# Performance work log

Measured on AMD Instinct MI355X. Metric: run time of the kernel, lower is better.

The kernel has to match this reference:

```python
import jax, jax.numpy as jnp
import numpy as np

B = 2097152
CXR, ECG, EHR = 15, 14, 13
TOTAL = CXR + ECG + EHR  # 42
LN_EPS = 1e-5


def setup_inputs() -> dict:
    key = jax.random.key(0)
    ks = jax.random.split(key, 40)
    f32 = jnp.float32
    inp = {
        "cxr_probs": jax.random.normal(ks[0], (B, CXR), dtype=f32),
        "ecg_probs": jax.random.normal(ks[1], (B, ECG), dtype=f32),
        "ehr_probs": jax.random.normal(ks[2], (B, EHR), dtype=f32),
    }
    for i, (name, E) in enumerate([("cxr", CXR), ("ecg", ECG), ("ehr", EHR)]):
        k0 = 3 + i * 8
        s_in = 1.0 / np.sqrt(E)
        s_kv = 1.0 / np.sqrt(TOTAL)
        inp[f"in_w_{name}"] = jax.random.normal(ks[k0], (3 * E, E), dtype=f32) * s_in
        inp[f"in_b_{name}"] = jnp.zeros((3 * E,), dtype=f32)
        inp[f"out_w_{name}"] = jax.random.normal(ks[k0 + 1], (E, E), dtype=f32) * s_in
        inp[f"out_b_{name}"] = jnp.zeros((E,), dtype=f32)
        inp[f"kv_w_{name}"] = jax.random.normal(ks[k0 + 2], (E, TOTAL), dtype=f32) * s_kv
        inp[f"kv_b_{name}"] = jax.random.normal(ks[k0 + 3], (E,), dtype=f32) * s_kv
        inp[f"ln_g_{name}"] = jnp.ones((E,), dtype=f32)
        inp[f"ln_b_{name}"] = jnp.zeros((E,), dtype=f32)
    return inp


def _branch(x, ctx, in_w, in_b, out_w, out_b, kv_w, kv_b, ln_g, ln_b):
    # x: [B, E], ctx: [B, 42]
    E = x.shape[-1]
    kv = ctx @ kv_w.T + kv_b                      # [B, E]
    # nn.MultiheadAttention with q_len = kv_len = 1: softmax over a single
    # key is identically 1, so attn_out == v_proj(kv) exactly.
    Wv, bv = in_w[2 * E:], in_b[2 * E:]
    v = kv @ Wv.T + bv                            # [B, E]
    attended = v @ out_w.T + out_b                # [B, E]
    y = x + attended
    mu = jnp.mean(y, axis=-1, keepdims=True)
    var = jnp.mean(jnp.square(y - mu), axis=-1, keepdims=True)
    return (y - mu) * jax.lax.rsqrt(var + LN_EPS) * ln_g + ln_b


def reference(cxr_probs, ecg_probs, ehr_probs,
              in_w_cxr, in_b_cxr, out_w_cxr, out_b_cxr, kv_w_cxr, kv_b_cxr, ln_g_cxr, ln_b_cxr,
              in_w_ecg, in_b_ecg, out_w_ecg, out_b_ecg, kv_w_ecg, kv_b_ecg, ln_g_ecg, ln_b_ecg,
              in_w_ehr, in_b_ehr, out_w_ehr, out_b_ehr, kv_w_ehr, kv_b_ehr, ln_g_ehr, ln_b_ehr):
    ctx = jnp.concatenate([cxr_probs, ecg_probs, ehr_probs], axis=1)  # [B, 42]
    cxr_out = _branch(cxr_probs, ctx, in_w_cxr, in_b_cxr, out_w_cxr, out_b_cxr,
                      kv_w_cxr, kv_b_cxr, ln_g_cxr, ln_b_cxr)
    ecg_out = _branch(ecg_probs, ctx, in_w_ecg, in_b_ecg, out_w_ecg, out_b_ecg,
                      kv_w_ecg, kv_b_ecg, ln_g_ecg, ln_b_ecg)
    ehr_out = _branch(ehr_probs, ctx, in_w_ehr, in_b_ehr, out_w_ehr, out_b_ehr,
                      kv_w_ehr, kv_b_ehr, ln_g_ehr, ln_b_ehr)
    return (cxr_out, ecg_out, ehr_out)
```

## Files before the change

### kernel.cpp

```cpp
#include <hip/hip_runtime.h>
#include <stdint.h>

constexpr int CXR = 15, ECG = 14, EHR = 13;
constexpr int TOTAL = 42;
constexpr int MPITCH = 44;
constexpr float LN_EPS = 1e-5f;

constexpr int WS_M    = 0;
constexpr int WS_B    = TOTAL * MPITCH;
constexpr int WS_G    = WS_B + TOTAL;
constexpr int WS_BETA = WS_G + TOTAL;
constexpr int WS_FLOATS = WS_BETA + TOTAL;

constexpr int WROWS = 64;
constexpr int WFLOATS = WROWS * TOTAL;
constexpr int WS0F = 0;
constexpr int WS1F = WROWS * CXR;
constexpr int WS2F = WS1F + WROWS * ECG;
constexpr int WC0 = WROWS * CXR / 4;
constexpr int WC1 = WROWS * ECG / 4;
constexpr int WC2 = WROWS * EHR / 4;

typedef float f2v __attribute__((ext_vector_type(2)));
typedef __attribute__((address_space(4))) const f2v   CF2;
typedef __attribute__((address_space(4))) const float CFc;

__device__ __forceinline__ CF2* cast2(const float* p) {
    return (CF2*)(unsigned long long)p;
}
__device__ __forceinline__ CFc* cast1(const float* p) {
    return (CFc*)(unsigned long long)p;
}

struct FuseArgs {
    const float *in_w, *in_b, *out_w, *out_b, *kv_w, *kv_b, *ln_g, *ln_b;
    int E, R;
};

__global__ void fuse_weights_kernel(FuseArgs a0, FuseArgs a1, FuseArgs a2,
                                    float* __restrict__ ws) {
    FuseArgs a = (blockIdx.x == 0) ? a0 : (blockIdx.x == 1 ? a1 : a2);
    const int E = a.E, R = a.R;
    const int tid = threadIdx.x;

    __shared__ float T1[15 * 42];
    __shared__ float b1[15];

    for (int idx = tid; idx < E * TOTAL; idx += blockDim.x) {
        int i = idx / TOTAL, j = idx % TOTAL;
        float acc = 0.f;
        for (int k = 0; k < E; ++k)
            acc = fmaf(a.in_w[(2 * E + i) * E + k], a.kv_w[k * TOTAL + j], acc);
        T1[i * TOTAL + j] = acc;
    }
    if (tid < E) {
        float acc = a.in_b[2 * E + tid];
        for (int k = 0; k < E; ++k)
            acc = fmaf(a.in_w[(2 * E + tid) * E + k], a.kv_b[k], acc);
        b1[tid] = acc;
    }
    __syncthreads();

    for (int idx = tid; idx < E * MPITCH; idx += blockDim.x) {
        int i = idx / MPITCH, j = idx % MPITCH;
        float acc = 0.f;
        if (j < TOTAL)
            for (int k = 0; k < E; ++k)
                acc = fmaf(a.out_w[i * E + k], T1[k * TOTAL + j], acc);
        ws[WS_M + (R + i) * MPITCH + j] = acc;
    }
    if (tid < E) {
        float acc = a.out_b[tid];
        for (int k = 0; k < E; ++k)
            acc = fmaf(a.out_w[tid * E + k], b1[k], acc);
        ws[WS_B + R + tid]    = acc;
        ws[WS_G + R + tid]    = a.ln_g[tid];
        ws[WS_BETA + R + tid] = a.ln_b[tid];
    }
}

template <int CH>
__device__ __forceinline__ void stage_wave(const float* __restrict__ g,
                                           float* lds_seg_base, int lane) {
#pragma unroll
    for (int it = 0; it < (CH + 63) / 64; ++it) {
        int idx = lane + it * 64;
        if (idx < CH) {
            const __attribute__((address_space(1))) void* src =
                (const __attribute__((address_space(1))) void*)
                    ((const char*)g + (size_t)idx * 16);
            __attribute__((address_space(3))) void* dst =
                (__attribute__((address_space(3))) void*)
                    ((char*)lds_seg_base + it * 1024);
            __builtin_amdgcn_global_load_lds(src, dst, 16, 0, 0);
        }
    }
}

template <int E, int R, int SF>
__device__ __forceinline__ void compute_seg(const f2v (&ctx2)[MPITCH / 2],
                                            const float* __restrict__ ws,
                                            float* __restrict__ wb, int lane) {
    const float* ctxs = (const float*)ctx2;
    float y[E];
#pragma unroll
    for (int i = 0; i < E; ++i) {
        CF2* wrow = cast2(ws + WS_M + (R + i) * MPITCH);
        f2v acc = { *cast1(ws + WS_B + R + i), 0.f };
#pragma unroll
        for (int q = 0; q < MPITCH / 2; ++q) {
            f2v w = wrow[q];
            acc = __builtin_elementwise_fma(w, ctx2[q], acc);
        }
        y[i] = ctxs[R + i] + acc.x + acc.y;
    }
    float mu = 0.f;
#pragma unroll
    for (int i = 0; i < E; ++i) mu += y[i];
    mu *= (1.0f / E);
    float var = 0.f;
#pragma unroll
    for (int i = 0; i < E; ++i) { float d = y[i] - mu; var = fmaf(d, d, var); }
    var *= (1.0f / E);
    float rs = rsqrtf(var + LN_EPS);
#pragma unroll
    for (int i = 0; i < E; ++i) {
        float n = (y[i] - mu) * rs;
        wb[SF + lane * E + i] = fmaf(n, *cast1(ws + WS_G + R + i),
                                     *cast1(ws + WS_BETA + R + i));
    }
}

__global__ __launch_bounds__(128) void cmca_main(
        const float* __restrict__ cxr, const float* __restrict__ ecg,
        const float* __restrict__ ehr, const float* __restrict__ ws,
        float* __restrict__ out_cxr, float* __restrict__ out_ecg,
        float* __restrict__ out_ehr) {
    __shared__ __align__(16) float sbuf[2 * WFLOATS];
    const int tid = threadIdx.x;
    const int w = tid >> 6;
    const int lane = tid & 63;
    const size_t gw = (size_t)blockIdx.x * 2 + w;

    float* wb = sbuf + w * WFLOATS;

    const float* g0 = cxr + gw * (size_t)(WROWS * CXR);
    const float* g1 = ecg + gw * (size_t)(WROWS * ECG);
    const float* g2 = ehr + gw * (size_t)(WROWS * EHR);

    stage_wave<WC0>(g0, wb + WS0F, lane);
    stage_wave<WC1>(g1, wb + WS1F, lane);
    stage_wave<WC2>(g2, wb + WS2F, lane);
    asm volatile("s_waitcnt vmcnt(0)" ::: "memory");

    f2v ctx2[MPITCH / 2];
    float* ctxs = (float*)ctx2;
#pragma unroll
    for (int j = 0; j < CXR; ++j) ctxs[j] = wb[WS0F + lane * CXR + j];
#pragma unroll
    for (int j = 0; j < ECG; ++j) ctxs[CXR + j] = wb[WS1F + lane * ECG + j];
#pragma unroll
    for (int j = 0; j < EHR; ++j) ctxs[CXR + ECG + j] = wb[WS2F + lane * EHR + j];
    ctxs[42] = 0.f;
    ctxs[43] = 0.f;

    compute_seg<CXR, 0, WS0F>(ctx2, ws, wb, lane);
    compute_seg<ECG, CXR, WS1F>(ctx2, ws, wb, lane);
    compute_seg<EHR, CXR + ECG, WS2F>(ctx2, ws, wb, lane);

    const float4* wb4 = (const float4*)wb;
    float4* o0 = (float4*)(out_cxr + gw * (size_t)(WROWS * CXR));
    float4* o1 = (float4*)(out_ecg + gw * (size_t)(WROWS * ECG));
    float4* o2 = (float4*)(out_ehr + gw * (size_t)(WROWS * EHR));
#pragma unroll
    for (int it = 0; it < 4; ++it) {
        int idx = lane + it * 64;
        if (idx < WC0) o0[idx] = wb4[idx];
    }
#pragma unroll
    for (int it = 0; it < 4; ++it) {
        int idx = lane + it * 64;
        if (idx < WC1) o1[idx] = wb4[WC0 + idx];
    }
#pragma unroll
    for (int it = 0; it < 4; ++it) {
        int idx = lane + it * 64;
        if (idx < WC2) o2[idx] = wb4[WC0 + WC1 + idx];
    }
}

extern "C" void kernel_launch(void* const* d_in, const int* in_sizes, int n_in,
                              void* d_out, int out_size, void* d_ws, size_t ws_size,
                              hipStream_t stream) {
    const float* cxr = (const float*)d_in[0];
    const float* ecg = (const float*)d_in[1];
    const float* ehr = (const float*)d_in[2];
    float* ws = (float*)d_ws;
    float* out = (float*)d_out;

    const size_t Bn = (size_t)in_sizes[0] / CXR;

    auto mk = [&](int base, int E, int R) {
        FuseArgs a;
        a.in_w  = (const float*)d_in[base + 0];
        a.in_b  = (const float*)d_in[base + 1];
        a.out_w = (const float*)d_in[base + 2];
        a.out_b = (const float*)d_in[base + 3];
        a.kv_w  = (const float*)d_in[base + 4];
        a.kv_b  = (const float*)d_in[base + 5];
        a.ln_g  = (const float*)d_in[base + 6];
        a.ln_b  = (const float*)d_in[base + 7];
        a.E = E; a.R = R;
        return a;
    };
    FuseArgs a0 = mk(3, CXR, 0);
    FuseArgs a1 = mk(11, ECG, CXR);
    FuseArgs a2 = mk(19, EHR, CXR + ECG);

    fuse_weights_kernel<<<3, 256, 0, stream>>>(a0, a1, a2, ws);

    const int nblocks = (int)(Bn / (WROWS * 2));
    cmca_main<<<nblocks, 128, 0, stream>>>(cxr, ecg, ehr, ws,
                                           out,
                                           out + Bn * CXR,
                                           out + Bn * (CXR + ECG));
}
```

Measured before the change: 172.3 us.

## Compute fused 42x42 projection with fp16 MFMA instead of scalar FMAs

Adds a small kernel that packs the fused weight matrix, plus identity residual and bias row, into fp16 MFMA B-fragments. The main kernel converts each wave's 64 input rows to fp16 in a swizzled LDS arena and runs 16x16x32 f16 MFMAs. Accumulators are staged back through LDS for per-row LayerNorm. This removes the per-lane scalar FMA loop with its constant-memory weight reads, at the cost of fp16 rounding of inputs and weights, which risks accuracy, and extra LDS round-trips.

```diff
diff --git a/kernel.cpp b/kernel.cpp
--- a/kernel.cpp
+++ b/kernel.cpp
@@ -10,24 +10,16 @@
 constexpr int WS_B    = TOTAL * MPITCH;
 constexpr int WS_G    = WS_B + TOTAL;
 constexpr int WS_BETA = WS_G + TOTAL;
-constexpr int WS_FLOATS = WS_BETA + TOTAL;
+constexpr int WS_FRAG = 1976;
 
 constexpr int WROWS = 64;
-constexpr int WFLOATS = WROWS * TOTAL;
-constexpr int WS0F = 0;
-constexpr int WS1F = WROWS * CXR;
-constexpr int WS2F = WS1F + WROWS * ECG;
-constexpr int WC0 = WROWS * CXR / 4;
-constexpr int WC1 = WROWS * ECG / 4;
-constexpr int WC2 = WROWS * EHR / 4;
-
-typedef float f2v __attribute__((ext_vector_type(2)));
-typedef __attribute__((address_space(4))) const f2v   CF2;
+constexpr int ARENA_B = 11264;
+constexpr int S0F = 0, S1F = WROWS * CXR, S2F = S1F + WROWS * ECG;
+constexpr int WC0 = WROWS * CXR / 4, WC1 = WROWS * ECG / 4, WC2 = WROWS * EHR / 4;
+
+typedef _Float16 half8 __attribute__((ext_vector_type(8)));
+typedef float float4v __attribute__((ext_vector_type(4)));
 typedef __attribute__((address_space(4))) const float CFc;
-
-__device__ __forceinline__ CF2* cast2(const float* p) {
-    return (CF2*)(unsigned long long)p;
-}
 __device__ __forceinline__ CFc* cast1(const float* p) {
     return (CFc*)(unsigned long long)p;
 }
@@ -77,6 +69,31 @@
         ws[WS_G + R + tid]    = a.ln_g[tid];
         ws[WS_BETA + R + tid] = a.ln_b[tid];
     }
+}
+
+__global__ void fuse_frags_kernel(float* __restrict__ ws) {
+    const int tid = threadIdx.x;
+    if (tid >= 384) return;
+    const int l = tid & 63, nt = tid >> 6;
+    const int n = nt >> 1, t = nt & 1;
+    const int col = n * 16 + (l & 15);
+    const int k0 = t * 32 + 8 * (l >> 4);
+    half8 h;
+#pragma unroll
+    for (int i = 0; i < 8; ++i) {
+        int k = k0 + i;
+        float v = 0.f;
+        if (col < TOTAL) {
+            if (k < TOTAL) {
+                v = ws[WS_M + col * MPITCH + k];
+                if (k == col) v += 1.f;
+            } else if (k == TOTAL) {
+                v = ws[WS_B + col];
+            }
+        }
+        h[i] = (_Float16)v;
+    }
+    ((half8*)(ws + WS_FRAG))[nt * 64 + l] = h;
 }
 
 template <int CH>
@@ -97,81 +114,140 @@
     }
 }
 
-template <int E, int R, int SF>
-__device__ __forceinline__ void compute_seg(const f2v (&ctx2)[MPITCH / 2],
-                                            const float* __restrict__ ws,
-                                            float* __restrict__ wb, int lane) {
-    const float* ctxs = (const float*)ctx2;
-    float y[E];
-#pragma unroll
-    for (int i = 0; i < E; ++i) {
-        CF2* wrow = cast2(ws + WS_M + (R + i) * MPITCH);
-        f2v acc = { *cast1(ws + WS_B + R + i), 0.f };
-#pragma unroll
-        for (int q = 0; q < MPITCH / 2; ++q) {
-            f2v w = wrow[q];
-            acc = __builtin_elementwise_fma(w, ctx2[q], acc);
-        }
-        y[i] = ctxs[R + i] + acc.x + acc.y;
-    }
-    float mu = 0.f;
-#pragma unroll
-    for (int i = 0; i < E; ++i) mu += y[i];
-    mu *= (1.0f / E);
-    float var = 0.f;
-#pragma unroll
-    for (int i = 0; i < E; ++i) { float d = y[i] - mu; var = fmaf(d, d, var); }
-    var *= (1.0f / E);
-    float rs = rsqrtf(var + LN_EPS);
-#pragma unroll
-    for (int i = 0; i < E; ++i) {
-        float n = (y[i] - mu) * rs;
-        wb[SF + lane * E + i] = fmaf(n, *cast1(ws + WS_G + R + i),
-                                     *cast1(ws + WS_BETA + R + i));
-    }
-}
-
 __global__ __launch_bounds__(128) void cmca_main(
         const float* __restrict__ cxr, const float* __restrict__ ecg,
         const float* __restrict__ ehr, const float* __restrict__ ws,
         float* __restrict__ out_cxr, float* __restrict__ out_ecg,
         float* __restrict__ out_ehr) {
-    __shared__ __align__(16) float sbuf[2 * WFLOATS];
+    __shared__ __align__(16) char smem[2 * ARENA_B];
     const int tid = threadIdx.x;
-    const int w = tid >> 6;
-    const int lane = tid & 63;
+    const int w = tid >> 6, lane = tid & 63;
+    char* arena = smem + w * ARENA_B;
+    float* af = (float*)arena;
     const size_t gw = (size_t)blockIdx.x * 2 + w;
 
-    float* wb = sbuf + w * WFLOATS;
-
-    const float* g0 = cxr + gw * (size_t)(WROWS * CXR);
-    const float* g1 = ecg + gw * (size_t)(WROWS * ECG);
-    const float* g2 = ehr + gw * (size_t)(WROWS * EHR);
-
-    stage_wave<WC0>(g0, wb + WS0F, lane);
-    stage_wave<WC1>(g1, wb + WS1F, lane);
-    stage_wave<WC2>(g2, wb + WS2F, lane);
+    const half8* fr = (const half8*)(ws + WS_FRAG);
+    half8 bfrag[6];
+#pragma unroll
+    for (int q = 0; q < 6; ++q) bfrag[q] = fr[q * 64 + lane];
+
+    stage_wave<WC0>(cxr + gw * (size_t)(WROWS * CXR), af + S0F, lane);
+    stage_wave<WC1>(ecg + gw * (size_t)(WROWS * ECG), af + S1F, lane);
+    stage_wave<WC2>(ehr + gw * (size_t)(WROWS * EHR), af + S2F, lane);
     asm volatile("s_waitcnt vmcnt(0)" ::: "memory");
 
-    f2v ctx2[MPITCH / 2];
-    float* ctxs = (float*)ctx2;
-#pragma unroll
-    for (int j = 0; j < CXR; ++j) ctxs[j] = wb[WS0F + lane * CXR + j];
-#pragma unroll
-    for (int j = 0; j < ECG; ++j) ctxs[CXR + j] = wb[WS1F + lane * ECG + j];
-#pragma unroll
-    for (int j = 0; j < EHR; ++j) ctxs[CXR + ECG + j] = wb[WS2F + lane * EHR + j];
-    ctxs[42] = 0.f;
-    ctxs[43] = 0.f;
-
-    compute_seg<CXR, 0, WS0F>(ctx2, ws, wb, lane);
-    compute_seg<ECG, CXR, WS1F>(ctx2, ws, wb, lane);
-    compute_seg<EHR, CXR + ECG, WS2F>(ctx2, ws, wb, lane);
-
-    const float4* wb4 = (const float4*)wb;
-    float4* o0 = (float4*)(out_cxr + gw * (size_t)(WROWS * CXR));
-    float4* o1 = (float4*)(out_ecg + gw * (size_t)(WROWS * ECG));
-    float4* o2 = (float4*)(out_ehr + gw * (size_t)(WROWS * EHR));
+    float x[TOTAL];
+#pragma unroll
+    for (int j = 0; j < CXR; ++j) x[j] = af[S0F + lane * CXR + j];
+#pragma unroll
+    for (int j = 0; j < ECG; ++j) x[CXR + j] = af[S1F + lane * ECG + j];
+#pragma unroll
+    for (int j = 0; j < EHR; ++j) x[CXR + ECG + j] = af[S2F + lane * EHR + j];
+    __builtin_amdgcn_sched_barrier(0);
+
+    {
+        const int swz = (lane & 7) << 4;
+#pragma unroll
+        for (int j = 0; j < 8; ++j) {
+            half8 h;
+#pragma unroll
+            for (int e = 0; e < 8; ++e) {
+                int idx = j * 8 + e;
+                float v = (idx < TOTAL) ? x[idx] : (idx == TOTAL ? 1.f : 0.f);
+                h[e] = (_Float16)v;
+            }
+            *(half8*)(arena + ((lane * 128 + j * 16) ^ swz)) = h;
+        }
+    }
+    __builtin_amdgcn_sched_barrier(0);
+
+    half8 afr[4][2];
+#pragma unroll
+    for (int m = 0; m < 4; ++m) {
+        int row = m * 16 + (lane & 15);
+        int rswz = (row & 7) << 4;
+#pragma unroll
+        for (int t = 0; t < 2; ++t)
+            afr[m][t] = *(const half8*)(arena +
+                ((row * 128 + t * 64 + (lane >> 4) * 16) ^ rswz));
+    }
+    __builtin_amdgcn_sched_barrier(0);
+
+    float4v acc[4][3];
+#pragma unroll
+    for (int m = 0; m < 4; ++m)
+#pragma unroll
+        for (int n = 0; n < 3; ++n) acc[m][n] = float4v{0.f, 0.f, 0.f, 0.f};
+#pragma unroll
+    for (int t = 0; t < 2; ++t)
+#pragma unroll
+        for (int m = 0; m < 4; ++m)
+#pragma unroll
+            for (int n = 0; n < 3; ++n)
+                acc[m][n] = __builtin_amdgcn_mfma_f32_16x16x32_f16(
+                    afr[m][t], bfrag[n * 2 + t], acc[m][n], 0, 0, 0);
+
+    __builtin_amdgcn_sched_barrier(0);
+#pragma unroll
+    for (int m = 0; m < 4; ++m)
+#pragma unroll
+        for (int n = 0; n < 3; ++n)
+#pragma unroll
+            for (int r = 0; r < 4; ++r) {
+                int row = m * 16 + (lane >> 4) * 4 + r;
+                int col = n * 16 + (lane & 15);
+                if (col < MPITCH) af[row * MPITCH + col] = acc[m][n][r];
+            }
+    __builtin_amdgcn_sched_barrier(0);
+
+    float y[MPITCH];
+#pragma unroll
+    for (int j = 0; j < 11; ++j) {
+        float4v q = *(const float4v*)(af + lane * MPITCH + j * 4);
+        y[j * 4 + 0] = q[0]; y[j * 4 + 1] = q[1];
+        y[j * 4 + 2] = q[2]; y[j * 4 + 3] = q[3];
+    }
+    __builtin_amdgcn_sched_barrier(0);
+
+    float res[TOTAL];
+    {
+#define LN_SEG(S, E)                                                       \
+        {                                                                  \
+            float mu = 0.f;                                                \
+            _Pragma("unroll")                                              \
+            for (int i = 0; i < (E); ++i) mu += y[(S) + i];                \
+            mu *= (1.0f / (E));                                            \
+            float var = 0.f;                                               \
+            _Pragma("unroll")                                              \
+            for (int i = 0; i < (E); ++i) {                                \
+                float d = y[(S) + i] - mu; var = fmaf(d, d, var);          \
+            }                                                              \
+            var *= (1.0f / (E));                                           \
+            float rs = rsqrtf(var + LN_EPS);                               \
+            _Pragma("unroll")                                              \
+            for (int i = 0; i < (E); ++i) {                                \
+                float nv = (y[(S) + i] - mu) * rs;                         \
+                res[(S) + i] = fmaf(nv, *cast1(ws + WS_G + (S) + i),       \
+                                    *cast1(ws + WS_BETA + (S) + i));       \
+            }                                                              \
+        }
+        LN_SEG(0, CXR)
+        LN_SEG(CXR, ECG)
+        LN_SEG(CXR + ECG, EHR)
+#undef LN_SEG
+    }
+#pragma unroll
+    for (int j = 0; j < CXR; ++j) af[S0F + lane * CXR + j] = res[j];
+#pragma unroll
+    for (int j = 0; j < ECG; ++j) af[S1F + lane * ECG + j] = res[CXR + j];
+#pragma unroll
+    for (int j = 0; j < EHR; ++j) af[S2F + lane * EHR + j] = res[CXR + ECG + j];
+    __builtin_amdgcn_sched_barrier(0);
+
+    const float4v* wb4 = (const float4v*)af;
+    float4v* o0 = (float4v*)(out_cxr + gw * (size_t)(WROWS * CXR));
+    float4v* o1 = (float4v*)(out_ecg + gw * (size_t)(WROWS * ECG));
+    float4v* o2 = (float4v*)(out_ehr + gw * (size_t)(WROWS * EHR));
 #pragma unroll
     for (int it = 0; it < 4; ++it) {
         int idx = lane + it * 64;
@@ -218,6 +294,7 @@
     FuseArgs a2 = mk(19, EHR, CXR + ECG);
 
     fuse_weights_kernel<<<3, 256, 0, stream>>>(a0, a1, a2, ws);
+    fuse_frags_kernel<<<1, 384, 0, stream>>>(ws);
 
     const int nblocks = (int)(Bn / (WROWS * 2));
     cmca_main<<<nblocks, 128, 0, stream>>>(cxr, ecg, ehr, ws,
```

New measurement: 146.5 us. 1.18x faster.
